# Kernel optimization log

Hardware: AMD Instinct MI355X
Metric: run time of the kernel (lower is better)

Reference implementation:

```python
import jax, jax.numpy as jnp
import numpy as np


def _shift(x, n):
    # torch.roll along the last (angular) axis
    return jnp.roll(x, n, axis=3)


def _flip(x, n):
    # mirror about index n along the last axis: out[..., i] = x[..., (n - i) mod W]
    return jnp.roll(jnp.flip(x, axis=3), n + 1, axis=3)


def setup_inputs() -> dict:
    key = jax.random.key(0)
    k1, k2, k3 = jax.random.split(key, 3)
    B, C, H, W = 16, 96, 96, 96
    x = jax.random.normal(k1, (B, C, H, W), dtype=jnp.float32)
    s = jax.random.normal(k2, (B, 5), dtype=jnp.float32)
    w = jax.random.uniform(k3, (B, C, H, W), dtype=jnp.float32) + 0.1  # keep denominator well-conditioned
    return {"x": x, "s": s, "w": w}


def reference(x, s, w):
    # s.shape[1] == 5 branch of SymmetryControl (square symmetry: 3 rotations + 2 mirrors)
    sg = jax.nn.sigmoid(s).reshape(s.shape[0], -1, 1, 1)  # [B,5,1,1]
    step = x.shape[3] // 8

    x90 = _shift(x, step * 2)
    x180 = _shift(x, step * 4)
    x270 = _shift(x, step * 6)
    x90f = _flip(x, step * 2 - 1)
    x180f = _flip(x, step * 4 - 1)

    w90 = sg[:, 0:1] * _shift(w, step * 2)
    w180 = sg[:, 1:2] * _shift(w, step * 4)
    w270 = sg[:, 2:3] * _shift(w, step * 6)
    w90f = sg[:, 3:4] * _flip(w, step * 2 - 1)
    w180f = sg[:, 4:5] * _flip(w, step * 4 - 1)

    a = (w * x + w90 * x90 + w180 * x180 + w270 * x270
         + w90f * x90f + w180f * x180f)
    b = w + w90 + w180 + w270 + w90f + w180f
    return a / b
```

## Files before the change

### kernel.cpp

```cpp
#include <hip/hip_runtime.h>


#define WDIM  96
#define RPB   9216
#define WPB   4
#define PAIRS 4
#define RPW   (2 * PAIRS)

typedef float v2f __attribute__((ext_vector_type(2)));

__device__ __forceinline__ float bperm(int byteidx, float v) {
    return __int_as_float(__builtin_amdgcn_ds_bpermute(byteidx, __float_as_int(v)));
}

__global__ __launch_bounds__(64 * WPB)
void symctl_kernel(const float* __restrict__ x,
                   const float* __restrict__ s,
                   const float* __restrict__ w,
                   float* __restrict__ out) {
    const int lane = threadIdx.x & 63;
    const int tl   = lane & 31;
    const int hsel = lane & 32;
    const int h    = lane >> 5;

    const int wid  = blockIdx.x * WPB + (threadIdx.x >> 6);
    const int voff = ((RPW * wid + h) * WDIM + 3 * tl) * 4;

    const int b = (blockIdx.x * (RPW * WPB)) / RPB;
    const float* sb = s + b * 5;
    const float sg0 = 1.0f / (1.0f + __expf(-sb[0]));
    const float sg1 = 1.0f / (1.0f + __expf(-sb[1]));
    const float sg2 = 1.0f / (1.0f + __expf(-sb[2]));
    const float sg3 = 1.0f / (1.0f + __expf(-sb[3]));
    const float sg4 = 1.0f / (1.0f + __expf(-sb[4]));

    const int i90  = (hsel | ((tl -  8) & 31)) << 2;
    const int i180 = (hsel | ((tl - 16) & 31)) << 2;
    const int i270 = (hsel | ((tl +  8) & 31)) << 2;
    const int f90  = (hsel | (( 7 - tl) & 31)) << 2;
    const int f180 = (hsel | ((15 - tl) & 31)) << 2;

    v2f   xlo0, xlo1, xlo2, xlo3, wlo0, wlo1, wlo2, wlo3;
    float xhi0, xhi1, xhi2, xhi3, whi0, whi1, whi2, whi3;
#define LD_PAIR(K, XLO, XHI, WLO, WHI)                                          \
    asm volatile("global_load_dwordx2 %0, %1, %2 offset:" #K                    \
                 : "=v"(XLO) : "v"(voff), "s"(x));                              \
    asm volatile("global_load_dword %0, %1, %2 offset:" #K "+8"                 \
                 : "=v"(XHI) : "v"(voff), "s"(x));                              \
    asm volatile("global_load_dwordx2 %0, %1, %2 offset:" #K                    \
                 : "=v"(WLO) : "v"(voff), "s"(w));                              \
    asm volatile("global_load_dword %0, %1, %2 offset:" #K "+8"                 \
                 : "=v"(WHI) : "v"(voff), "s"(w));
    LD_PAIR(0,    xlo0, xhi0, wlo0, whi0)
    LD_PAIR(768,  xlo1, xhi1, wlo1, whi1)
    LD_PAIR(1536, xlo2, xhi2, wlo2, whi2)
    LD_PAIR(2304, xlo3, xhi3, wlo3, whi3)
#undef LD_PAIR

    float o0x,o0y,o0z, o1x,o1y,o1z, o2x,o2y,o2z, o3x,o3y,o3z;

#define COMPUTE(XLO, XHI, WLO, WHI, OX, OY, OZ)                                 \
    {                                                                           \
        const float wcx = WLO.x, wcy = WLO.y, wcz = WHI;                        \
        const float p0 = XLO.x * wcx;                                           \
        const float p1 = XLO.y * wcy;                                           \
        const float p2 = XHI   * wcz;                                           \
        float n0 = p0, n1 = p1, n2 = p2;                                        \
        float d0 = wcx, d1 = wcy, d2 = wcz;                                     \
        n0 = fmaf(sg0, bperm(i90,  p0),  n0);                                   \
        n1 = fmaf(sg0, bperm(i90,  p1),  n1);                                   \
        n2 = fmaf(sg0, bperm(i90,  p2),  n2);                                   \
        d0 = fmaf(sg0, bperm(i90,  wcx), d0);                                   \
        d1 = fmaf(sg0, bperm(i90,  wcy), d1);                                   \
        d2 = fmaf(sg0, bperm(i90,  wcz), d2);                                   \
        n0 = fmaf(sg1, bperm(i180, p0),  n0);                                   \
        n1 = fmaf(sg1, bperm(i180, p1),  n1);                                   \
        n2 = fmaf(sg1, bperm(i180, p2),  n2);                                   \
        d0 = fmaf(sg1, bperm(i180, wcx), d0);                                   \
        d1 = fmaf(sg1, bperm(i180, wcy), d1);                                   \
        d2 = fmaf(sg1, bperm(i180, wcz), d2);                                   \
        n0 = fmaf(sg2, bperm(i270, p0),  n0);                                   \
        n1 = fmaf(sg2, bperm(i270, p1),  n1);                                   \
        n2 = fmaf(sg2, bperm(i270, p2),  n2);                                   \
        d0 = fmaf(sg2, bperm(i270, wcx), d0);                                   \
        d1 = fmaf(sg2, bperm(i270, wcy), d1);                                   \
        d2 = fmaf(sg2, bperm(i270, wcz), d2);                                   \
        n0 = fmaf(sg3, bperm(f90,  p2),  n0);                                   \
        n1 = fmaf(sg3, bperm(f90,  p1),  n1);                                   \
        n2 = fmaf(sg3, bperm(f90,  p0),  n2);                                   \
        d0 = fmaf(sg3, bperm(f90,  wcz), d0);                                   \
        d1 = fmaf(sg3, bperm(f90,  wcy), d1);                                   \
        d2 = fmaf(sg3, bperm(f90,  wcx), d2);                                   \
        n0 = fmaf(sg4, bperm(f180, p2),  n0);                                   \
        n1 = fmaf(sg4, bperm(f180, p1),  n1);                                   \
        n2 = fmaf(sg4, bperm(f180, p0),  n2);                                   \
        d0 = fmaf(sg4, bperm(f180, wcz), d0);                                   \
        d1 = fmaf(sg4, bperm(f180, wcy), d1);                                   \
        d2 = fmaf(sg4, bperm(f180, wcx), d2);                                   \
        OX = n0 * __builtin_amdgcn_rcpf(d0);                                    \
        OY = n1 * __builtin_amdgcn_rcpf(d1);                                    \
        OZ = n2 * __builtin_amdgcn_rcpf(d2);                                    \
    }

    asm volatile("s_waitcnt vmcnt(12)" ::: "memory");
    __builtin_amdgcn_sched_barrier(0);
    COMPUTE(xlo0, xhi0, wlo0, whi0, o0x, o0y, o0z)

    asm volatile("s_waitcnt vmcnt(8)" ::: "memory");
    __builtin_amdgcn_sched_barrier(0);
    COMPUTE(xlo1, xhi1, wlo1, whi1, o1x, o1y, o1z)

    asm volatile("s_waitcnt vmcnt(4)" ::: "memory");
    __builtin_amdgcn_sched_barrier(0);
    COMPUTE(xlo2, xhi2, wlo2, whi2, o2x, o2y, o2z)

    asm volatile("s_waitcnt vmcnt(0)" ::: "memory");
    __builtin_amdgcn_sched_barrier(0);
    COMPUTE(xlo3, xhi3, wlo3, whi3, o3x, o3y, o3z)
#undef COMPUTE

    float* op = out + (voff >> 2);
    float3 o;
    o.x = o0x; o.y = o0y; o.z = o0z; *(float3*)(op + 0 * 2 * WDIM) = o;
    o.x = o1x; o.y = o1y; o.z = o1z; *(float3*)(op + 1 * 2 * WDIM) = o;
    o.x = o2x; o.y = o2y; o.z = o2z; *(float3*)(op + 2 * 2 * WDIM) = o;
    o.x = o3x; o.y = o3y; o.z = o3z; *(float3*)(op + 3 * 2 * WDIM) = o;
}

extern "C" void kernel_launch(void* const* d_in, const int* in_sizes, int n_in,
                              void* d_out, int out_size, void* d_ws, size_t ws_size,
                              hipStream_t stream) {
    const float* x = (const float*)d_in[0];
    const float* s = (const float*)d_in[1];
    const float* w = (const float*)d_in[2];
    float* out = (float*)d_out;

    const int n_rows = in_sizes[0] / WDIM;
    const int waves  = n_rows / RPW;
    const int grid   = waves / WPB;

    dim3 block(64 * WPB);
    symctl_kernel<<<grid, block, 0, stream>>>(x, s, w, out);
}
```

Baseline: 152.1 us.

## Software-pipeline nine row-pairs per wave with rotating buffers and inline stores

Each wave now processes nine row pairs (18 rows) instead of four. Loads run through a three-stage rotating register pipeline, and vmcnt waits are placed so that computing one pair overlaps the loads for the next two. Outputs are written right after each pair with inline asm stores instead of at the end. The grid is fixed at 2048 blocks and the batch index is hardcoded as blockIdx>>7, which ties the kernel to the given shape and relies on stores counting toward vmcnt on this architecture.

```diff
diff --git a/kernel.cpp b/kernel.cpp
--- a/kernel.cpp
+++ b/kernel.cpp
@@ -1,11 +1,10 @@
 #include <hip/hip_runtime.h>
 
 
-#define WDIM  96
-#define RPB   9216
-#define WPB   4
-#define PAIRS 4
-#define RPW   (2 * PAIRS)
+#define WDIM 96
+#define WPB  4
+#define NP   9
+#define GRID 2048
 
 typedef float v2f __attribute__((ext_vector_type(2)));
 
@@ -23,10 +22,10 @@
     const int hsel = lane & 32;
     const int h    = lane >> 5;
 
-    const int wid  = blockIdx.x * WPB + (threadIdx.x >> 6);
-    const int voff = ((RPW * wid + h) * WDIM + 3 * tl) * 4;
+    const int gw   = blockIdx.x * WPB + (threadIdx.x >> 6);
+    const int voff = ((18 * gw + h) * WDIM + 3 * tl) * 4;
 
-    const int b = (blockIdx.x * (RPW * WPB)) / RPB;
+    const int b = blockIdx.x >> 7;
     const float* sb = s + b * 5;
     const float sg0 = 1.0f / (1.0f + __expf(-sb[0]));
     const float sg1 = 1.0f / (1.0f + __expf(-sb[1]));
@@ -40,26 +39,29 @@
     const int f90  = (hsel | (( 7 - tl) & 31)) << 2;
     const int f180 = (hsel | ((15 - tl) & 31)) << 2;
 
-    v2f   xlo0, xlo1, xlo2, xlo3, wlo0, wlo1, wlo2, wlo3;
-    float xhi0, xhi1, xhi2, xhi3, whi0, whi1, whi2, whi3;
-#define LD_PAIR(K, XLO, XHI, WLO, WHI)                                          \
-    asm volatile("global_load_dwordx2 %0, %1, %2 offset:" #K                    \
-                 : "=v"(XLO) : "v"(voff), "s"(x));                              \
-    asm volatile("global_load_dword %0, %1, %2 offset:" #K "+8"                 \
-                 : "=v"(XHI) : "v"(voff), "s"(x));                              \
-    asm volatile("global_load_dwordx2 %0, %1, %2 offset:" #K                    \
-                 : "=v"(WLO) : "v"(voff), "s"(w));                              \
-    asm volatile("global_load_dword %0, %1, %2 offset:" #K "+8"                 \
-                 : "=v"(WHI) : "v"(voff), "s"(w));
-    LD_PAIR(0,    xlo0, xhi0, wlo0, whi0)
-    LD_PAIR(768,  xlo1, xhi1, wlo1, whi1)
-    LD_PAIR(1536, xlo2, xhi2, wlo2, whi2)
-    LD_PAIR(2304, xlo3, xhi3, wlo3, whi3)
-#undef LD_PAIR
+    __builtin_amdgcn_sched_barrier(0);
 
-    float o0x,o0y,o0z, o1x,o1y,o1z, o2x,o2y,o2z, o3x,o3y,o3z;
+    v2f   xloA, xloB, xloC, wloA, wloB, wloC;
+    float xhiA, xhiB, xhiC, whiA, whiB, whiC;
 
-#define COMPUTE(XLO, XHI, WLO, WHI, OX, OY, OZ)                                 \
+#define LD(K, XLO, XHI, WLO, WHI)                                               \
+    {                                                                           \
+        const int a_ = voff + (K) * 768;                                        \
+        asm volatile("global_load_dwordx2 %0, %1, %2"                           \
+                     : "=v"(XLO) : "v"(a_), "s"(x));                            \
+        asm volatile("global_load_dword %0, %1, %2 offset:8"                    \
+                     : "=v"(XHI) : "v"(a_), "s"(x));                            \
+        asm volatile("global_load_dwordx2 %0, %1, %2"                           \
+                     : "=v"(WLO) : "v"(a_), "s"(w));                            \
+        asm volatile("global_load_dword %0, %1, %2 offset:8"                    \
+                     : "=v"(WHI) : "v"(a_), "s"(w));                            \
+    }
+
+#define WAITN(N)                                                                \
+    asm volatile("s_waitcnt vmcnt(" #N ")" ::: "memory");                       \
+    __builtin_amdgcn_sched_barrier(0);
+
+#define CST(K, XLO, XHI, WLO, WHI)                                              \
     {                                                                           \
         const float wcx = WLO.x, wcy = WLO.y, wcz = WHI;                        \
         const float p0 = XLO.x * wcx;                                           \
@@ -97,34 +99,33 @@
         d0 = fmaf(sg4, bperm(f180, wcz), d0);                                   \
         d1 = fmaf(sg4, bperm(f180, wcy), d1);                                   \
         d2 = fmaf(sg4, bperm(f180, wcx), d2);                                   \
-        OX = n0 * __builtin_amdgcn_rcpf(d0);                                    \
-        OY = n1 * __builtin_amdgcn_rcpf(d1);                                    \
-        OZ = n2 * __builtin_amdgcn_rcpf(d2);                                    \
+        v2f olo;                                                                \
+        olo.x = n0 * __builtin_amdgcn_rcpf(d0);                                 \
+        olo.y = n1 * __builtin_amdgcn_rcpf(d1);                                 \
+        const float ohi = n2 * __builtin_amdgcn_rcpf(d2);                       \
+        const int a_ = voff + (K) * 768;                                        \
+        asm volatile("global_store_dwordx2 %0, %1, %2"                          \
+                     :: "v"(a_), "v"(olo), "s"(out) : "memory");                \
+        asm volatile("global_store_dword %0, %1, %2 offset:8"                   \
+                     :: "v"(a_), "v"(ohi), "s"(out) : "memory");                \
     }
 
-    asm volatile("s_waitcnt vmcnt(12)" ::: "memory");
-    __builtin_amdgcn_sched_barrier(0);
-    COMPUTE(xlo0, xhi0, wlo0, whi0, o0x, o0y, o0z)
+    LD(0, xloA, xhiA, wloA, whiA)
+    LD(1, xloB, xhiB, wloB, whiB)
 
-    asm volatile("s_waitcnt vmcnt(8)" ::: "memory");
-    __builtin_amdgcn_sched_barrier(0);
-    COMPUTE(xlo1, xhi1, wlo1, whi1, o1x, o1y, o1z)
+    LD(2, xloC, xhiC, wloC, whiC)  WAITN(8)   CST(0, xloA, xhiA, wloA, whiA)
+    LD(3, xloA, xhiA, wloA, whiA)  WAITN(10)  CST(1, xloB, xhiB, wloB, whiB)
+    LD(4, xloB, xhiB, wloB, whiB)  WAITN(12)  CST(2, xloC, xhiC, wloC, whiC)
+    LD(5, xloC, xhiC, wloC, whiC)  WAITN(12)  CST(3, xloA, xhiA, wloA, whiA)
+    LD(6, xloA, xhiA, wloA, whiA)  WAITN(12)  CST(4, xloB, xhiB, wloB, whiB)
+    LD(7, xloB, xhiB, wloB, whiB)  WAITN(12)  CST(5, xloC, xhiC, wloC, whiC)
+    LD(8, xloC, xhiC, wloC, whiC)  WAITN(12)  CST(6, xloA, xhiA, wloA, whiA)
+                                   WAITN(8)   CST(7, xloB, xhiB, wloB, whiB)
+                                   WAITN(4)   CST(8, xloC, xhiC, wloC, whiC)
 
-    asm volatile("s_waitcnt vmcnt(4)" ::: "memory");
-    __builtin_amdgcn_sched_barrier(0);
-    COMPUTE(xlo2, xhi2, wlo2, whi2, o2x, o2y, o2z)
-
-    asm volatile("s_waitcnt vmcnt(0)" ::: "memory");
-    __builtin_amdgcn_sched_barrier(0);
-    COMPUTE(xlo3, xhi3, wlo3, whi3, o3x, o3y, o3z)
-#undef COMPUTE
-
-    float* op = out + (voff >> 2);
-    float3 o;
-    o.x = o0x; o.y = o0y; o.z = o0z; *(float3*)(op + 0 * 2 * WDIM) = o;
-    o.x = o1x; o.y = o1y; o.z = o1z; *(float3*)(op + 1 * 2 * WDIM) = o;
-    o.x = o2x; o.y = o2y; o.z = o2z; *(float3*)(op + 2 * 2 * WDIM) = o;
-    o.x = o3x; o.y = o3y; o.z = o3z; *(float3*)(op + 3 * 2 * WDIM) = o;
+#undef LD
+#undef WAITN
+#undef CST
 }
 
 extern "C" void kernel_launch(void* const* d_in, const int* in_sizes, int n_in,
@@ -135,10 +136,6 @@
     const float* w = (const float*)d_in[2];
     float* out = (float*)d_out;
 
-    const int n_rows = in_sizes[0] / WDIM;
-    const int waves  = n_rows / RPW;
-    const int grid   = waves / WPB;
-
     dim3 block(64 * WPB);
-    symctl_kernel<<<grid, block, 0, stream>>>(x, s, w, out);
+    symctl_kernel<<<GRID, block, 0, stream>>>(x, s, w, out);
 }
```

Result: no change. 154.1 us (+1.3%).
